# Kernel tuning notes

Hardware: AMD Instinct MI355X
Metric: run time of the kernel (lower is better)

Reference implementation:

```python
import jax, jax.numpy as jnp
import numpy as np

B, S, D = 4, 2048, 512
H, DK, DV = 8, 64, 64


def setup_inputs() -> dict:
    key = jax.random.key(0)
    ks = jax.random.split(key, 12)
    inv = 1.0 / np.sqrt(D)
    return {
        "query": jax.random.normal(ks[0], (B, S, D), dtype=jnp.float32),
        "value": jax.random.normal(ks[1], (B, S, D), dtype=jnp.float32),
        "attention_mask": jax.random.randint(ks[2], (B, S), 0, 2, dtype=jnp.int32),
        "Wq": jax.random.normal(ks[3], (D, H * DK), dtype=jnp.float32) * inv,
        "bq": jnp.zeros((H * DK,), dtype=jnp.float32),
        "Wk": jax.random.normal(ks[4], (D, H * DK), dtype=jnp.float32) * inv,
        "bk": jnp.zeros((H * DK,), dtype=jnp.float32),
        "Wv": jax.random.normal(ks[5], (D, H * DV), dtype=jnp.float32) * inv,
        "bv": jnp.zeros((H * DV,), dtype=jnp.float32),
        "Wo": jax.random.normal(ks[6], (H * DV, D), dtype=jnp.float32) * inv,
        "bo": jnp.zeros((D,), dtype=jnp.float32),
    }


def _split_heads(x, h):
    b, s, _ = x.shape
    return x.reshape(b, s, h, -1).transpose(0, 2, 1, 3)  # (B,H,S,dh)


def reference(query, value, attention_mask, Wq, bq, Wk, bk, Wv, bv, Wo, bo):
    # QKV projections (activation=None -> identity); key defaults to value
    q = _split_heads(query @ Wq + bq, H)   # (B,H,S,DK)
    k = _split_heads(value @ Wk + bk, H)   # (B,H,S,DK)
    v = _split_heads(value @ Wv + bv, H)   # (B,H,S,DV)

    scores = jnp.einsum("bhqd,bhkd->bhqk", q, k) / jnp.sqrt(jnp.float32(DK))
    # additive mask: m = 1e9*(mask-1), applied on both key and query axes
    m = 1e9 * (attention_mask.astype(jnp.float32) - 1.0)  # (B,S)
    scores = scores + m[:, None, None, :] + m[:, None, :, None]

    weights = jax.nn.softmax(scores, axis=-1)
    ctx = jnp.einsum("bhqk,bhkd->bhqd", weights, v)        # (B,H,S,DV)
    ctx = ctx.transpose(0, 2, 1, 3).reshape(ctx.shape[0], ctx.shape[2], H * DV)
    return ctx @ Wo + bo  # (B,S,D)
```

## Files before the change

### kernel.cpp

```cpp
#include <hip/hip_runtime.h>

#define B_ 4
#define S_ 2048
#define D_ 512
#define H_ 8

typedef __attribute__((ext_vector_type(8))) __bf16 bf16x8;
typedef __attribute__((ext_vector_type(4))) float f32x4;

#define NEGBIG  -1.442695040e9f
#define QSCALE  0.18033688011112042f

__device__ __forceinline__ unsigned pack_rn(float a, float b) {
    union { float f; unsigned u; } ua, ub; ua.f = a; ub.f = b;
    return __builtin_amdgcn_perm(ub.u + 0x8000u, ua.u + 0x8000u, 0x07060302u);
}

__device__ __forceinline__ void gl16(const void* g, void* l) {
    __builtin_amdgcn_global_load_lds(
        (const __attribute__((address_space(1))) unsigned int*)g,
        (__attribute__((address_space(3))) unsigned int*)l, 16, 0, 0);
}

__global__ __launch_bounds__(256) void pre_all(
    const float* __restrict__ q, const float* __restrict__ v,
    const int* __restrict__ am,
    const float* __restrict__ Wq, const float* __restrict__ Wk,
    const float* __restrict__ Wv, const float* __restrict__ Wo,
    unsigned short* __restrict__ xq, unsigned short* __restrict__ xv,
    unsigned short* __restrict__ Tq, unsigned short* __restrict__ Tk,
    unsigned short* __restrict__ Tv, unsigned short* __restrict__ To,
    int* __restrict__ idxc, int* __restrict__ nvout,
    float* __restrict__ Mf, float* __restrict__ Mc)
{
    const int bid = blockIdx.x;
    const int tid = threadIdx.x;

    if (bid < 4096) {
        const int z = bid >> 11, xb = bid & 2047;
        const float* src = z ? v : q;
        unsigned short* dst = z ? xv : xq;
        int i = (xb * 256 + tid) * 8;
        float4 f0 = *(const float4*)&src[i];
        float4 f1 = *(const float4*)&src[i + 4];
        uint4 o;
        o.x = pack_rn(f0.x, f0.y); o.y = pack_rn(f0.z, f0.w);
        o.z = pack_rn(f1.x, f1.y); o.w = pack_rn(f1.z, f1.w);
        *(uint4*)&dst[i] = o;
    } else if (bid < 4352) {
        int r = bid - 4096;
        int z = r >> 6, rem = r & 63;
        const float* W = (z == 0) ? Wq : (z == 1) ? Wk : (z == 2) ? Wv : Wo;
        unsigned short* T = (z == 0) ? Tq : (z == 1) ? Tk : (z == 2) ? Tv : To;
        int n0 = (rem & 7) * 64, k0 = (rem >> 3) * 64;

        __shared__ float Ts[64][69];
        #pragma unroll
        for (int it = 0; it < 4; it++) {
            int lin = tid + it * 256;
            int kr = lin >> 4, c4 = (lin & 15) * 4;
            float4 vv = *(const float4*)&W[(k0 + kr) * 512 + n0 + c4];
            Ts[kr][c4 + 0] = vv.x; Ts[kr][c4 + 1] = vv.y;
            Ts[kr][c4 + 2] = vv.z; Ts[kr][c4 + 3] = vv.w;
        }
        __syncthreads();
        int n = tid >> 2, kc = tid & 3;
        unsigned p[8];
        #pragma unroll
        for (int j = 0; j < 8; j++)
            p[j] = pack_rn(Ts[kc * 16 + 2 * j][n], Ts[kc * 16 + 2 * j + 1][n]);
        unsigned short* dst = &T[(n0 + n) * 512 + k0 + kc * 16];
        *(uint4*)dst       = *(uint4*)&p[0];
        *(uint4*)(dst + 8) = *(uint4*)&p[4];
    } else {
        const int w = tid >> 6, lane = tid & 63;
        const int* amb = am + w * 2048;
        int m[32];
        #pragma unroll
        for (int s = 0; s < 32; s++) m[s] = amb[s * 64 + lane];

        int* ib = idxc + w * 2048;
        const unsigned long long lt = (1ULL << lane) - 1ULL;
        int base = 0;
        #pragma unroll
        for (int s = 0; s < 32; s++) {
            unsigned long long bal = __ballot(m[s] != 0);
            if (m[s]) ib[base + __popcll(bal & lt)] = s * 64 + lane;
            base += __popcll(bal);
        }
        const int nv = base;
        for (int i = nv + lane; i < 2048; i += 64) ib[i] = 0;
        float* mfb = Mf + w * 2048;
        float* mcb = Mc + w * 2048;
        #pragma unroll
        for (int s = 0; s < 32; s++) {
            int i = s * 64 + lane;
            mfb[i] = m[s] ? 0.f : NEGBIG;
            mcb[i] = (i < nv) ? 0.f : NEGBIG;
        }
        if (lane == 0) nvout[w] = nv;
    }
}

__global__ __launch_bounds__(256) void proj_qkv_mfma(
    const unsigned short* __restrict__ Xq, const unsigned short* __restrict__ Xv,
    const unsigned short* __restrict__ Wtq, const unsigned short* __restrict__ Wtk,
    const unsigned short* __restrict__ Wtv,
    const float* __restrict__ bq, const float* __restrict__ bk,
    const float* __restrict__ bv,
    const int* __restrict__ idxc, const int* __restrict__ nv1,
    unsigned short* __restrict__ Qb, unsigned short* __restrict__ Kb,
    unsigned short* __restrict__ VtG)
{
    const int z = blockIdx.z;
    const unsigned short* A  = (z == 0) ? Wtq : (z == 1) ? Wtk : Xv;
    const unsigned short* Bm = (z == 0) ? Xq  : (z == 1) ? Xv  : Wtv;
    const float* bias        = (z == 0) ? bq  : (z == 1) ? bk  : bv;
    const int lin0 = blockIdx.y * 128 + blockIdx.x;
    const int m0 = (z < 2) ? blockIdx.y * 128 : (lin0 >> 3) * 128;
    const int n0 = (z < 2) ? blockIdx.x * 64  : (lin0 & 7) * 64;

    if (z == 1) {
        int bb = n0 >> 11, cap = (nv1[bb] + 63) & ~63;
        if (cap < 64) cap = 64;
        if ((n0 & 2047) >= cap) return;
    }
    if (z == 2) {
        int bb = m0 >> 11, cap = (nv1[bb] + 63) & ~63;
        if (cap < 64) cap = 64;
        if ((m0 & 2047) >= cap) return;
    }

    const int tid = threadIdx.x;
    const int w = tid >> 6, lane = tid & 63;
    const int l15 = lane & 15, quad = lane >> 4;
    const int wm = (w >> 1) * 64, wn = (w & 1) * 32;

    __shared__ unsigned short As[2][128 * 64];
    __shared__ unsigned short Bs[2][64 * 64];

    const int srw  = tid >> 3;
    const int csrc = (tid & 7) ^ (srw & 7);
    const unsigned short* aS[4];
    const unsigned short* bS[2];
    #pragma unroll
    for (int is = 0; is < 4; is++) {
        int ra = m0 + is * 32 + srw;
        long sa = ra;
        if (z == 2) { int bb = ra >> 11; sa = (long)bb * 2048 + idxc[bb * 2048 + (ra & 2047)]; }
        aS[is] = A + sa * 512 + csrc * 8;
    }
    #pragma unroll
    for (int is = 0; is < 2; is++) {
        int rb = n0 + is * 32 + srw;
        long sb = rb;
        if (z == 1) { int bb = rb >> 11; sb = (long)bb * 2048 + idxc[bb * 2048 + (rb & 2047)]; }
        bS[is] = Bm + sb * 512 + csrc * 8;
    }

    const int koff0 = ((quad    ) ^ (l15 & 7)) * 8;
    const int koff1 = ((quad + 4) ^ (l15 & 7)) * 8;

    f32x4 acc[4][2];
    #pragma unroll
    for (int i = 0; i < 4; i++)
        #pragma unroll
        for (int j = 0; j < 2; j++) acc[i][j] = (f32x4){0.f, 0.f, 0.f, 0.f};

    #define STAGE_Q(buf, k0)                                        \
        do {                                                        \
            _Pragma("unroll")                                       \
            for (int is = 0; is < 4; is++)                          \
                gl16(aS[is] + (k0), &As[buf][is * 2048 + w * 512]); \
            _Pragma("unroll")                                       \
            for (int is = 0; is < 2; is++)                          \
                gl16(bS[is] + (k0), &Bs[buf][is * 2048 + w * 512]); \
        } while (0)

    STAGE_Q(0, 0);
    for (int k = 0; k < 8; k++) {
        const int cur = k & 1;
        if (k < 7) {
            STAGE_Q(cur ^ 1, (k + 1) * 64);
            asm volatile("s_waitcnt vmcnt(6)" ::: "memory");
        } else {
            asm volatile("s_waitcnt vmcnt(0)" ::: "memory");
        }
        asm volatile("s_barrier" ::: "memory");
        #pragma unroll
        for (int kc = 0; kc < 2; kc++) {
            const int ko = kc ? koff1 : koff0;
            bf16x8 a[4], bb[2];
            #pragma unroll
            for (int i = 0; i < 4; i++)
                a[i] = *(const bf16x8*)&As[cur][(wm + 16 * i + l15) * 64 + ko];
            #pragma unroll
            for (int j = 0; j < 2; j++)
                bb[j] = *(const bf16x8*)&Bs[cur][(wn + 16 * j + l15) * 64 + ko];
            #pragma unroll
            for (int i = 0; i < 4; i++)
                #pragma unroll
                for (int j = 0; j < 2; j++)
                    acc[i][j] = __builtin_amdgcn_mfma_f32_16x16x32_bf16(a[i], bb[j], acc[i][j], 0, 0, 0);
        }
        asm volatile("s_barrier" ::: "memory");
    }
    #undef STAGE_Q

    if (z == 2) {
        #pragma unroll
        for (int j = 0; j < 2; j++) {
            int N = n0 + wn + 16 * j + l15;
            float bv_ = bias[N];
            int h = N >> 6, d = N & 63;
            #pragma unroll
            for (int i = 0; i < 4; i++) {
                int Mb = m0 + wm + 16 * i + quad * 4;
                int b = Mb >> 11, s = Mb & 2047;
                uint2 o;
                o.x = pack_rn(acc[i][j][0] + bv_, acc[i][j][1] + bv_);
                o.y = pack_rn(acc[i][j][2] + bv_, acc[i][j][3] + bv_);
                *(uint2*)&VtG[((b * H_ + h) * 64 + d) * 2048 + s] = o;
            }
        }
    } else {
        unsigned short* dst = (z == 0) ? Qb : Kb;
        const float scale = (z == 0) ? QSCALE : 1.0f;
        #pragma unroll
        for (int j = 0; j < 2; j++) {
            int sg = n0 + wn + 16 * j + l15;
            int b = sg >> 11, s = sg & 2047;
            #pragma unroll
            for (int i = 0; i < 4; i++) {
                int F = m0 + wm + 16 * i + quad * 4;
                int h = F >> 6, d = F & 63;
                float4 b4 = *(const float4*)&bias[F];
                uint2 o;
                o.x = pack_rn((acc[i][j][0] + b4.x) * scale, (acc[i][j][1] + b4.y) * scale);
                o.y = pack_rn((acc[i][j][2] + b4.z) * scale, (acc[i][j][3] + b4.w) * scale);
                *(uint2*)&dst[((b * H_ + h) * 2048 + s) * 64 + d] = o;
            }
        }
    }
}

__global__ __launch_bounds__(256, 2) void flash_mfma(
    const unsigned short* __restrict__ Qg, const unsigned short* __restrict__ Kg,
    const unsigned short* __restrict__ VtG, const float* __restrict__ Mf,
    const float* __restrict__ Mc, const int* __restrict__ nvalid,
    unsigned short* __restrict__ ctxB)
{
    const int bid = blockIdx.x;
    const int xcd = bid & 7, idx = bid >> 3;
    const int bh = xcd * 4 + (idx & 3);
    const int q0 = (idx >> 2) * 128;
    const int b = bh >> 3, h = bh & 7;

    const int tid = threadIdx.x;
    const int w = tid >> 6, lane = tid & 63;
    const int l15 = lane & 15, quad = lane >> 4;
    const int swz = l15 & 7;

    __shared__ unsigned short Ks[2][64 * 64];
    __shared__ unsigned short Ps[4][32 * 64];
    unsigned short* pw = &Ps[w][0];

    const int nv = nvalid[b];
    int ntiles = (nv + 63) >> 6;
    if (ntiles < 1) ntiles = 1;

    const float* mfb = Mf + b * 2048;
    const float* mcp = Mc + b * 2048 + quad * 4;

    bf16x8 qf[2][2];
    float mq[2];
    #pragma unroll
    for (int qb = 0; qb < 2; qb++) {
        int qrow = q0 + w * 32 + qb * 16 + l15;
        const unsigned short* p = &Qg[((long)bh * 2048 + qrow) * 64 + quad * 8];
        qf[qb][0] = *(const bf16x8*)p;
        qf[qb][1] = *(const bf16x8*)(p + 32);
        mq[qb] = mfb[qrow];
    }

    const unsigned short* vp[4];
    #pragma unroll
    for (int i = 0; i < 4; i++)
        vp[i] = VtG + ((long)bh * 64 + i * 16 + l15) * 2048 + quad * 8;

    const int srow = tid >> 2;
    const int sch  = (tid & 3) * 2;
    const unsigned short* kgb = Kg + (long)bh * 2048 * 64;
    const int sw0 = srow * 64 + ((sch    ) ^ (srow & 7)) * 8;
    const int sw1 = srow * 64 + ((sch + 1) ^ (srow & 7)) * 8;

    {
        uint4 a = *(const uint4*)&kgb[srow * 64 + sch * 8];
        uint4 c = *(const uint4*)&kgb[srow * 64 + sch * 8 + 8];
        *(uint4*)&Ks[0][sw0] = a;
        *(uint4*)&Ks[0][sw1] = c;
    }
    const int kt1 = (ntiles > 1) ? 64 : 0;
    uint4 kstA = *(const uint4*)&kgb[(kt1 + srow) * 64 + sch * 8];
    uint4 kstB = *(const uint4*)&kgb[(kt1 + srow) * 64 + sch * 8 + 8];

    const int koff0 = ((quad    ) ^ swz) * 8;
    const int koff1 = ((quad + 4) ^ swz) * 8;

    f32x4 accO[2][4];
    #pragma unroll
    for (int qb = 0; qb < 2; qb++)
        #pragma unroll
        for (int dt = 0; dt < 4; dt++) accO[qb][dt] = (f32x4){0.f, 0.f, 0.f, 0.f};
    float mi[2] = {-3.0e38f, -3.0e38f};
    float li[2] = {0.f, 0.f};

    __syncthreads();

    f32x4 scA[2][4], scB[2][4];
    {
        f32x4 kmf[4];
        #pragma unroll
        for (int nt = 0; nt < 4; nt++)
            kmf[nt] = *(const f32x4*)(mcp + nt * 16);
        bf16x8 kf[4][2];
        #pragma unroll
        for (int nt = 0; nt < 4; nt++) {
            kf[nt][0] = *(const bf16x8*)&Ks[0][(nt * 16 + l15) * 64 + koff0];
            kf[nt][1] = *(const bf16x8*)&Ks[0][(nt * 16 + l15) * 64 + koff1];
        }
        #pragma unroll
        for (int qb = 0; qb < 2; qb++)
            #pragma unroll
            for (int nt = 0; nt < 4; nt++) {
                f32x4 c = kmf[nt];
                c[0] += mq[qb]; c[1] += mq[qb]; c[2] += mq[qb]; c[3] += mq[qb];
                c = __builtin_amdgcn_mfma_f32_16x16x32_bf16(kf[nt][0], qf[qb][0], c, 0, 0, 0);
                c = __builtin_amdgcn_mfma_f32_16x16x32_bf16(kf[nt][1], qf[qb][1], c, 0, 0, 0);
                scA[qb][nt] = c;
            }
    }

    auto STEP = [&](f32x4 (&scCur)[2][4], f32x4 (&scNxt)[2][4], int t) {
        const int kt = t * 64;
        const int n = (t & 1) ^ 1;
        const bool hasNext = (t + 1 < ntiles);
        const int kt2 = (t + 2 < ntiles) ? (t + 2) * 64 : (ntiles - 1) * 64;

        bf16x8 vf[4][2];
        #pragma unroll
        for (int dt = 0; dt < 4; dt++) {
            vf[dt][0] = *(const bf16x8*)(vp[dt] + kt);
            vf[dt][1] = *(const bf16x8*)(vp[dt] + kt + 32);
        }
        uint4 k2A = *(const uint4*)&kgb[(kt2 + srow) * 64 + sch * 8];
        uint4 k2B = *(const uint4*)&kgb[(kt2 + srow) * 64 + sch * 8 + 8];
        f32x4 kmf[4];
        #pragma unroll
        for (int nt = 0; nt < 4; nt++)
            kmf[nt] = *(const f32x4*)(mcp + kt + 64 + nt * 16);

        *(uint4*)&Ks[n][sw0] = kstA;
        *(uint4*)&Ks[n][sw1] = kstB;
        __syncthreads();
        kstA = k2A; kstB = k2B;

        if (hasNext) {
            bf16x8 kf[4][2];
            #pragma unroll
            for (int nt = 0; nt < 4; nt++) {
                kf[nt][0] = *(const bf16x8*)&Ks[n][(nt * 16 + l15) * 64 + koff0];
                kf[nt][1] = *(const bf16x8*)&Ks[n][(nt * 16 + l15) * 64 + koff1];
            }
            #pragma unroll
            for (int qb = 0; qb < 2; qb++)
                #pragma unroll
                for (int nt = 0; nt < 4; nt++) {
                    f32x4 c = kmf[nt];
                    c[0] += mq[qb]; c[1] += mq[qb]; c[2] += mq[qb]; c[3] += mq[qb];
                    c = __builtin_amdgcn_mfma_f32_16x16x32_bf16(kf[nt][0], qf[qb][0], c, 0, 0, 0);
                    c = __builtin_amdgcn_mfma_f32_16x16x32_bf16(kf[nt][1], qf[qb][1], c, 0, 0, 0);
                    scNxt[qb][nt] = c;
                }
        }

        #pragma unroll
        for (int qb = 0; qb < 2; qb++) {
            float mloc = fmaxf(fmaxf(scCur[qb][0][0], scCur[qb][0][1]),
                               fmaxf(scCur[qb][0][2], scCur[qb][0][3]));
            #pragma unroll
            for (int nt = 1; nt < 4; nt++)
                mloc = fmaxf(mloc, fmaxf(fmaxf(scCur[qb][nt][0], scCur[qb][nt][1]),
                                         fmaxf(scCur[qb][nt][2], scCur[qb][nt][3])));
            mloc = fmaxf(mloc, __shfl_xor(mloc, 16));
            mloc = fmaxf(mloc, __shfl_xor(mloc, 32));

            float mn = mi[qb];
            if (!__all(mloc <= mn + 4.f)) {
                float mo = mn;
                mn = fmaxf(mo, mloc);
                float alpha = __builtin_amdgcn_exp2f(mo - mn);
                li[qb] *= alpha;
                #pragma unroll
                for (int dt = 0; dt < 4; dt++) {
                    accO[qb][dt][0] *= alpha; accO[qb][dt][1] *= alpha;
                    accO[qb][dt][2] *= alpha; accO[qb][dt][3] *= alpha;
                }
                mi[qb] = mn;
            }

            float ps = 0.f;
            const int prbase = (qb * 16 + l15) * 64;
            #pragma unroll
            for (int nt = 0; nt < 4; nt++) {
                float p0 = __builtin_amdgcn_exp2f(scCur[qb][nt][0] - mn);
                float p1 = __builtin_amdgcn_exp2f(scCur[qb][nt][1] - mn);
                float p2 = __builtin_amdgcn_exp2f(scCur[qb][nt][2] - mn);
                float p3 = __builtin_amdgcn_exp2f(scCur[qb][nt][3] - mn);
                ps += (p0 + p1) + (p2 + p3);
                uint2 pp;
                pp.x = pack_rn(p0, p1);
                pp.y = pack_rn(p2, p3);
                *(uint2*)&pw[prbase + ((2 * nt + (quad >> 1)) ^ swz) * 8 + (quad & 1) * 4] = pp;
            }
            ps += __shfl_xor(ps, 16);
            ps += __shfl_xor(ps, 32);
            li[qb] += ps;
        }

        #pragma unroll
        for (int qb = 0; qb < 2; qb++) {
            bf16x8 pf0 = *(const bf16x8*)&pw[(qb * 16 + l15) * 64 + koff0];
            bf16x8 pf1 = *(const bf16x8*)&pw[(qb * 16 + l15) * 64 + koff1];
            __builtin_amdgcn_s_setprio(1);
            #pragma unroll
            for (int dt = 0; dt < 4; dt++) {
                accO[qb][dt] = __builtin_amdgcn_mfma_f32_16x16x32_bf16(
                    vf[dt][0], pf0, accO[qb][dt], 0, 0, 0);
                accO[qb][dt] = __builtin_amdgcn_mfma_f32_16x16x32_bf16(
                    vf[dt][1], pf1, accO[qb][dt], 0, 0, 0);
            }
            __builtin_amdgcn_s_setprio(0);
        }
    };

    for (int t = 0; t < ntiles; t += 2) {
        STEP(scA, scB, t);
        if (t + 1 < ntiles) STEP(scB, scA, t + 1);
    }

    #pragma unroll
    for (int qb = 0; qb < 2; qb++) {
        float inv = 1.f / li[qb];
        int q = q0 + w * 32 + qb * 16 + l15;
        int obase = (b * 2048 + q) * 512 + h * 64 + quad * 4;
        #pragma unroll
        for (int dt = 0; dt < 4; dt++) {
            uint2 o;
            o.x = pack_rn(accO[qb][dt][0] * inv, accO[qb][dt][1] * inv);
            o.y = pack_rn(accO[qb][dt][2] * inv, accO[qb][dt][3] * inv);
            *(uint2*)&ctxB[obase + dt * 16] = o;
        }
    }
}

__global__ __launch_bounds__(256) void proj_out_mfma(
    const unsigned short* __restrict__ ctxB, const unsigned short* __restrict__ Wto,
    const float* __restrict__ bo, float* __restrict__ out)
{
    const int m0 = blockIdx.y * 128, n0 = blockIdx.x * 64;
    const int tid = threadIdx.x;
    const int w = tid >> 6, lane = tid & 63;
    const int l15 = lane & 15, quad = lane >> 4;
    const int wm = (w >> 1) * 64, wn = (w & 1) * 32;

    __shared__ unsigned short As[2][128 * 64];
    __shared__ unsigned short Bs[2][64 * 64];

    const int srw  = tid >> 3;
    const int csrc = (tid & 7) ^ (srw & 7);
    const unsigned short* aS[4];
    const unsigned short* bS[2];
    #pragma unroll
    for (int is = 0; is < 4; is++)
        aS[is] = Wto  + (long)(m0 + is * 32 + srw) * 512 + csrc * 8;
    #pragma unroll
    for (int is = 0; is < 2; is++)
        bS[is] = ctxB + (long)(n0 + is * 32 + srw) * 512 + csrc * 8;

    const int koff0 = ((quad    ) ^ (l15 & 7)) * 8;
    const int koff1 = ((quad + 4) ^ (l15 & 7)) * 8;

    f32x4 acc[4][2];
    #pragma unroll
    for (int i = 0; i < 4; i++)
        #pragma unroll
        for (int j = 0; j < 2; j++) acc[i][j] = (f32x4){0.f, 0.f, 0.f, 0.f};

    #define STAGE_O(buf, k0)                                        \
        do {                                                        \
            _Pragma("unroll")                                       \
            for (int is = 0; is < 4; is++)                          \
                gl16(aS[is] + (k0), &As[buf][is * 2048 + w * 512]); \
            _Pragma("unroll")                                       \
            for (int is = 0; is < 2; is++)                          \
                gl16(bS[is] + (k0), &Bs[buf][is * 2048 + w * 512]); \
        } while (0)

    STAGE_O(0, 0);
    for (int k = 0; k < 8; k++) {
        const int cur = k & 1;
        if (k < 7) {
            STAGE_O(cur ^ 1, (k + 1) * 64);
            asm volatile("s_waitcnt vmcnt(6)" ::: "memory");
        } else {
            asm volatile("s_waitcnt vmcnt(0)" ::: "memory");
        }
        asm volatile("s_barrier" ::: "memory");
        #pragma unroll
        for (int kc = 0; kc < 2; kc++) {
            const int ko = kc ? koff1 : koff0;
            bf16x8 a[4], bb[2];
            #pragma unroll
            for (int i = 0; i < 4; i++)
                a[i] = *(const bf16x8*)&As[cur][(wm + 16 * i + l15) * 64 + ko];
            #pragma unroll
            for (int j = 0; j < 2; j++)
                bb[j] = *(const bf16x8*)&Bs[cur][(wn + 16 * j + l15) * 64 + ko];
            #pragma unroll
            for (int i = 0; i < 4; i++)
                #pragma unroll
                for (int j = 0; j < 2; j++)
                    acc[i][j] = __builtin_amdgcn_mfma_f32_16x16x32_bf16(a[i], bb[j], acc[i][j], 0, 0, 0);
        }
        asm volatile("s_barrier" ::: "memory");
    }
    #undef STAGE_O

    #pragma unroll
    for (int j = 0; j < 2; j++) {
        int sg = n0 + wn + 16 * j + l15;
        #pragma unroll
        for (int i = 0; i < 4; i++) {
            int F = m0 + wm + 16 * i + quad * 4;
            float4 b4 = *(const float4*)&bo[F];
            float4 vv;
            vv.x = acc[i][j][0] + b4.x;
            vv.y = acc[i][j][1] + b4.y;
            vv.z = acc[i][j][2] + b4.z;
            vv.w = acc[i][j][3] + b4.w;
            *(float4*)&out[sg * 512 + F] = vv;
        }
    }
}

extern "C" void kernel_launch(void* const* d_in, const int* in_sizes, int n_in,
                              void* d_out, int out_size, void* d_ws, size_t ws_size,
                              hipStream_t stream)
{
    const float* query = (const float*)d_in[0];
    const float* value = (const float*)d_in[1];
    const int*   amask = (const int*)d_in[2];
    const float* Wq = (const float*)d_in[3];
    const float* bq = (const float*)d_in[4];
    const float* Wk = (const float*)d_in[5];
    const float* bk = (const float*)d_in[6];
    const float* Wv = (const float*)d_in[7];
    const float* bv = (const float*)d_in[8];
    const float* Wo = (const float*)d_in[9];
    const float* bo = (const float*)d_in[10];
    float* out = (float*)d_out;

    char* ws = (char*)d_ws;
    const size_t MB = 1 << 20;
    const size_t KB = 1 << 10;
    unsigned short* Xbq = (unsigned short*)(ws);
    unsigned short* Xbv = (unsigned short*)(ws + 8 * MB);
    unsigned short* Wtq = (unsigned short*)(ws + 16 * MB);
    unsigned short* Wtk = (unsigned short*)(ws + 16 * MB + MB / 2);
    unsigned short* Wtv = (unsigned short*)(ws + 17 * MB);
    unsigned short* Wto = (unsigned short*)(ws + 17 * MB + MB / 2);
    unsigned short* Qb  = (unsigned short*)(ws + 18 * MB);
    unsigned short* Kb  = (unsigned short*)(ws + 26 * MB);
    unsigned short* VtG = (unsigned short*)(ws + 34 * MB);
    int*   idx1 = (int*)(ws + 42 * MB);
    float* Mf   = (float*)(ws + 42 * MB + 32 * KB);
    float* Mc   = (float*)(ws + 42 * MB + 64 * KB);
    int*   nv   = (int*)(ws + 42 * MB + 96 * KB);
    unsigned short* ctx = Xbq;

    pre_all<<<dim3(4353), 256, 0, stream>>>(query, value, amask,
                                            Wq, Wk, Wv, Wo,
                                            Xbq, Xbv, Wtq, Wtk, Wtv, Wto,
                                            idx1, nv, Mf, Mc);
    proj_qkv_mfma<<<dim3(128, 4, 3), 256, 0, stream>>>(Xbq, Xbv, Wtq, Wtk, Wtv,
                                                       bq, bk, bv, idx1, nv,
                                                       Qb, Kb, VtG);
    flash_mfma<<<dim3(512), 256, 0, stream>>>(Qb, Kb, VtG, Mf, Mc, nv, ctx);
    proj_out_mfma<<<dim3(128, 4), 256, 0, stream>>>(ctx, Wto, bo, out);
}
```

Before: 180.3 us.

## Fuse fp32-to-bf16 activation conversion into QKV projection GEMM staging

Drops the separate pass in the preprocessing kernel that converted query and value to bf16 in workspace. The QKV projection kernel now loads fp32 activations through registers, packs them to bf16 and writes them into swizzled LDS, while weight tiles keep using async global-to-LDS loads. This saves a full read/write round trip of the activations, but each GEMM block reads twice the bytes for activations and register-staged loads plus __syncthreads replace the async-copy waits.

```diff
diff --git a/kernel.cpp b/kernel.cpp
--- a/kernel.cpp
+++ b/kernel.cpp
@@ -22,12 +22,10 @@
         (__attribute__((address_space(3))) unsigned int*)l, 16, 0, 0);
 }
 
-__global__ __launch_bounds__(256) void pre_all(
-    const float* __restrict__ q, const float* __restrict__ v,
+__global__ __launch_bounds__(256) void pre_small(
     const int* __restrict__ am,
     const float* __restrict__ Wq, const float* __restrict__ Wk,
     const float* __restrict__ Wv, const float* __restrict__ Wo,
-    unsigned short* __restrict__ xq, unsigned short* __restrict__ xv,
     unsigned short* __restrict__ Tq, unsigned short* __restrict__ Tk,
     unsigned short* __restrict__ Tv, unsigned short* __restrict__ To,
     int* __restrict__ idxc, int* __restrict__ nvout,
@@ -36,20 +34,8 @@
     const int bid = blockIdx.x;
     const int tid = threadIdx.x;
 
-    if (bid < 4096) {
-        const int z = bid >> 11, xb = bid & 2047;
-        const float* src = z ? v : q;
-        unsigned short* dst = z ? xv : xq;
-        int i = (xb * 256 + tid) * 8;
-        float4 f0 = *(const float4*)&src[i];
-        float4 f1 = *(const float4*)&src[i + 4];
-        uint4 o;
-        o.x = pack_rn(f0.x, f0.y); o.y = pack_rn(f0.z, f0.w);
-        o.z = pack_rn(f1.x, f1.y); o.w = pack_rn(f1.z, f1.w);
-        *(uint4*)&dst[i] = o;
-    } else if (bid < 4352) {
-        int r = bid - 4096;
-        int z = r >> 6, rem = r & 63;
+    if (bid < 256) {
+        int z = bid >> 6, rem = bid & 63;
         const float* W = (z == 0) ? Wq : (z == 1) ? Wk : (z == 2) ? Wv : Wo;
         unsigned short* T = (z == 0) ? Tq : (z == 1) ? Tk : (z == 2) ? Tv : To;
         int n0 = (rem & 7) * 64, k0 = (rem >> 3) * 64;
@@ -103,7 +89,7 @@
 }
 
 __global__ __launch_bounds__(256) void proj_qkv_mfma(
-    const unsigned short* __restrict__ Xq, const unsigned short* __restrict__ Xv,
+    const float* __restrict__ Xqf, const float* __restrict__ Xvf,
     const unsigned short* __restrict__ Wtq, const unsigned short* __restrict__ Wtk,
     const unsigned short* __restrict__ Wtv,
     const float* __restrict__ bq, const float* __restrict__ bk,
@@ -113,9 +99,7 @@
     unsigned short* __restrict__ VtG)
 {
     const int z = blockIdx.z;
-    const unsigned short* A  = (z == 0) ? Wtq : (z == 1) ? Wtk : Xv;
-    const unsigned short* Bm = (z == 0) ? Xq  : (z == 1) ? Xv  : Wtv;
-    const float* bias        = (z == 0) ? bq  : (z == 1) ? bk  : bv;
+    const float* bias = (z == 0) ? bq : (z == 1) ? bk : bv;
     const int lin0 = blockIdx.y * 128 + blockIdx.x;
     const int m0 = (z < 2) ? blockIdx.y * 128 : (lin0 >> 3) * 128;
     const int n0 = (z < 2) ? blockIdx.x * 64  : (lin0 & 7) * 64;
@@ -141,22 +125,53 @@
 
     const int srw  = tid >> 3;
     const int csrc = (tid & 7) ^ (srw & 7);
-    const unsigned short* aS[4];
-    const unsigned short* bS[2];
-    #pragma unroll
-    for (int is = 0; is < 4; is++) {
-        int ra = m0 + is * 32 + srw;
-        long sa = ra;
-        if (z == 2) { int bb = ra >> 11; sa = (long)bb * 2048 + idxc[bb * 2048 + (ra & 2047)]; }
-        aS[is] = A + sa * 512 + csrc * 8;
-    }
-    #pragma unroll
-    for (int is = 0; is < 2; is++) {
-        int rb = n0 + is * 32 + srw;
-        long sb = rb;
-        if (z == 1) { int bb = rb >> 11; sb = (long)bb * 2048 + idxc[bb * 2048 + (rb & 2047)]; }
-        bS[is] = Bm + sb * 512 + csrc * 8;
-    }
+    const unsigned short* gS[4];
+    unsigned short* gD[2][4];
+    int ngl;
+    if (z < 2) {
+        const unsigned short* Wt = (z == 0) ? Wtq : Wtk;
+        #pragma unroll
+        for (int is = 0; is < 4; is++) {
+            gS[is] = Wt + (long)(m0 + is * 32 + srw) * 512 + csrc * 8;
+            gD[0][is] = &As[0][is * 2048 + w * 512];
+            gD[1][is] = &As[1][is * 2048 + w * 512];
+        }
+        ngl = 4;
+    } else {
+        #pragma unroll
+        for (int is = 0; is < 2; is++) {
+            gS[is] = Wtv + (long)(n0 + is * 32 + srw) * 512 + csrc * 8;
+            gD[0][is] = &Bs[0][is * 2048 + w * 512];
+            gD[1][is] = &Bs[1][is * 2048 + w * 512];
+        }
+        gS[2] = gS[0]; gS[3] = gS[0];
+        gD[0][2] = gD[0][0]; gD[0][3] = gD[0][0];
+        gD[1][2] = gD[1][0]; gD[1][3] = gD[1][0];
+        ngl = 2;
+    }
+
+    const float* xsrc;
+    int xrow, cbase, nch;
+    if (z < 2) {
+        int rx = n0 + (tid >> 2);
+        long s = rx;
+        if (z == 1) { int bb = rx >> 11; s = (long)bb * 2048 + idxc[bb * 2048 + (rx & 2047)]; }
+        xsrc = ((z == 0) ? Xqf : Xvf) + s * 512;
+        xrow = tid >> 2; cbase = (tid & 3) * 2; nch = 2;
+    } else {
+        int rx = m0 + (tid >> 1);
+        int bb = rx >> 11;
+        long s = (long)bb * 2048 + idxc[bb * 2048 + (rx & 2047)];
+        xsrc = Xvf + s * 512;
+        xrow = tid >> 1; cbase = (tid & 1) * 4; nch = 4;
+    }
+    int xw[4];
+    #pragma unroll
+    for (int j = 0; j < 4; j++)
+        xw[j] = xrow * 64 + (((cbase + j) & 7) ^ (xrow & 7)) * 8;
+    unsigned short* xD[2];
+    xD[0] = (z < 2) ? &Bs[0][0] : &As[0][0];
+    xD[1] = (z < 2) ? &Bs[1][0] : &As[1][0];
 
     const int koff0 = ((quad    ) ^ (l15 & 7)) * 8;
     const int koff1 = ((quad + 4) ^ (l15 & 7)) * 8;
@@ -167,26 +182,43 @@
         #pragma unroll
         for (int j = 0; j < 2; j++) acc[i][j] = (f32x4){0.f, 0.f, 0.f, 0.f};
 
-    #define STAGE_Q(buf, k0)                                        \
-        do {                                                        \
-            _Pragma("unroll")                                       \
-            for (int is = 0; is < 4; is++)                          \
-                gl16(aS[is] + (k0), &As[buf][is * 2048 + w * 512]); \
-            _Pragma("unroll")                                       \
-            for (int is = 0; is < 2; is++)                          \
-                gl16(bS[is] + (k0), &Bs[buf][is * 2048 + w * 512]); \
-        } while (0)
-
-    STAGE_Q(0, 0);
+    float4 xr[4][2];
+
+    #pragma unroll
+    for (int j = 0; j < 4; j++)
+        if (j < nch) {
+            xr[j][0] = *(const float4*)(xsrc + (cbase + j) * 8);
+            xr[j][1] = *(const float4*)(xsrc + (cbase + j) * 8 + 4);
+        }
+    #pragma unroll
+    for (int is = 0; is < 4; is++)
+        if (is < ngl) gl16(gS[is], gD[0][is]);
+    #pragma unroll
+    for (int j = 0; j < 4; j++)
+        if (j < nch) {
+            uint4 p;
+            p.x = pack_rn(xr[j][0].x, xr[j][0].y);
+            p.y = pack_rn(xr[j][0].z, xr[j][0].w);
+            p.z = pack_rn(xr[j][1].x, xr[j][1].y);
+            p.w = pack_rn(xr[j][1].z, xr[j][1].w);
+            *(uint4*)&xD[0][xw[j]] = p;
+        }
+    __syncthreads();
+
     for (int k = 0; k < 8; k++) {
-        const int cur = k & 1;
+        const int cur = k & 1, nxt = cur ^ 1;
         if (k < 7) {
-            STAGE_Q(cur ^ 1, (k + 1) * 64);
-            asm volatile("s_waitcnt vmcnt(6)" ::: "memory");
-        } else {
-            asm volatile("s_waitcnt vmcnt(0)" ::: "memory");
-        }
-        asm volatile("s_barrier" ::: "memory");
+            const int k1 = (k + 1) * 64;
+            #pragma unroll
+            for (int j = 0; j < 4; j++)
+                if (j < nch) {
+                    xr[j][0] = *(const float4*)(xsrc + k1 + (cbase + j) * 8);
+                    xr[j][1] = *(const float4*)(xsrc + k1 + (cbase + j) * 8 + 4);
+                }
+            #pragma unroll
+            for (int is = 0; is < 4; is++)
+                if (is < ngl) gl16(gS[is] + k1, gD[nxt][is]);
+        }
         #pragma unroll
         for (int kc = 0; kc < 2; kc++) {
             const int ko = kc ? koff1 : koff0;
@@ -203,9 +235,20 @@
                 for (int j = 0; j < 2; j++)
                     acc[i][j] = __builtin_amdgcn_mfma_f32_16x16x32_bf16(a[i], bb[j], acc[i][j], 0, 0, 0);
         }
-        asm volatile("s_barrier" ::: "memory");
-    }
-    #undef STAGE_Q
+        if (k < 7) {
+            #pragma unroll
+            for (int j = 0; j < 4; j++)
+                if (j < nch) {
+                    uint4 p;
+                    p.x = pack_rn(xr[j][0].x, xr[j][0].y);
+                    p.y = pack_rn(xr[j][0].z, xr[j][0].w);
+                    p.z = pack_rn(xr[j][1].x, xr[j][1].y);
+                    p.w = pack_rn(xr[j][1].z, xr[j][1].w);
+                    *(uint4*)&xD[nxt][xw[j]] = p;
+                }
+        }
+        __syncthreads();
+    }
 
     if (z == 2) {
         #pragma unroll
@@ -574,8 +617,7 @@
     char* ws = (char*)d_ws;
     const size_t MB = 1 << 20;
     const size_t KB = 1 << 10;
-    unsigned short* Xbq = (unsigned short*)(ws);
-    unsigned short* Xbv = (unsigned short*)(ws + 8 * MB);
+    unsigned short* ctx = (unsigned short*)(ws);
     unsigned short* Wtq = (unsigned short*)(ws + 16 * MB);
     unsigned short* Wtk = (unsigned short*)(ws + 16 * MB + MB / 2);
     unsigned short* Wtv = (unsigned short*)(ws + 17 * MB);
@@ -587,13 +629,12 @@
     float* Mf   = (float*)(ws + 42 * MB + 32 * KB);
     float* Mc   = (float*)(ws + 42 * MB + 64 * KB);
     int*   nv   = (int*)(ws + 42 * MB + 96 * KB);
-    unsigned short* ctx = Xbq;
-
-    pre_all<<<dim3(4353), 256, 0, stream>>>(query, value, amask,
-                                            Wq, Wk, Wv, Wo,
-                                            Xbq, Xbv, Wtq, Wtk, Wtv, Wto,
-                                            idx1, nv, Mf, Mc);
-    proj_qkv_mfma<<<dim3(128, 4, 3), 256, 0, stream>>>(Xbq, Xbv, Wtq, Wtk, Wtv,
+
+    pre_small<<<dim3(257), 256, 0, stream>>>(amask, Wq, Wk, Wv, Wo,
+                                             Wtq, Wtk, Wtv, Wto,
+                                             idx1, nv, Mf, Mc);
+    proj_qkv_mfma<<<dim3(128, 4, 3), 256, 0, stream>>>(query, value,
+                                                       Wtq, Wtk, Wtv,
                                                        bq, bk, bv, idx1, nv,
                                                        Qb, Kb, VtG);
     flash_mfma<<<dim3(512), 256, 0, stream>>>(Qb, Kb, VtG, Mf, Mc, nv, ctx);
```

Measured after the change: 190.2 us. +5.5%, slower.

## Fuse four attention kernels into one persistent kernel with grid barriers

Applied to the files above, without the earlier changes.

Merges the preprocessing, QKV projection, flash attention and output projection kernels into a single persistent kernel of 512 blocks. The phases are separated by software grid barriers built on atomic counters in workspace, which are zeroed with a memset before launch. The goal is to remove the per-launch overhead and tail gaps between the kernels. In exchange, all 512 blocks must be co-resident, since the spin barriers can deadlock if they are not. Shared memory is also unified into one 48 KB buffer, and the barriers add spin and fence costs.

```diff
diff --git a/kernel.cpp b/kernel.cpp
--- a/kernel.cpp
+++ b/kernel.cpp
@@ -22,22 +22,40 @@
         (__attribute__((address_space(3))) unsigned int*)l, 16, 0, 0);
 }
 
-__global__ __launch_bounds__(256) void pre_all(
-    const float* __restrict__ q, const float* __restrict__ v,
-    const int* __restrict__ am,
-    const float* __restrict__ Wq, const float* __restrict__ Wk,
-    const float* __restrict__ Wv, const float* __restrict__ Wo,
-    unsigned short* __restrict__ xq, unsigned short* __restrict__ xv,
-    unsigned short* __restrict__ Tq, unsigned short* __restrict__ Tk,
-    unsigned short* __restrict__ Tv, unsigned short* __restrict__ To,
-    int* __restrict__ idxc, int* __restrict__ nvout,
-    float* __restrict__ Mf, float* __restrict__ Mc)
+struct MegaArgs {
+    const float *q, *v; const int* am;
+    const float *Wq, *Wk, *Wv, *Wo, *bq, *bk, *bv, *bo;
+    unsigned short *Xbq, *Xbv, *Tq, *Tk, *Tv, *To;
+    unsigned short *Qb, *Kb, *VtG, *ctx;
+    int *idxc, *nv; float *Mf, *Mc; float* out;
+    unsigned* bars;
+};
+
+#define NBLK 512u
+
+__device__ __forceinline__ void grid_bar(unsigned* cnt) {
+    asm volatile("s_waitcnt vmcnt(0) lgkmcnt(0)" ::: "memory");
+    __syncthreads();
+    if (threadIdx.x == 0) {
+        __threadfence_system();
+        __hip_atomic_fetch_add(cnt, 1u, __ATOMIC_RELEASE, __HIP_MEMORY_SCOPE_AGENT);
+        while (__hip_atomic_load(cnt, __ATOMIC_ACQUIRE, __HIP_MEMORY_SCOPE_AGENT) < NBLK)
+            __builtin_amdgcn_s_sleep(2);
+        __threadfence_system();
+    }
+    __syncthreads();
+}
+
+__device__ void phase_pre(char* smem, int it,
+    const float* q, const float* v, const int* am,
+    const float* Wq, const float* Wk, const float* Wv, const float* Wo,
+    unsigned short* xq, unsigned short* xv,
+    unsigned short* Tq, unsigned short* Tk, unsigned short* Tv, unsigned short* To,
+    int* idxc, int* nvout, float* Mf, float* Mc)
 {
-    const int bid = blockIdx.x;
     const int tid = threadIdx.x;
-
-    if (bid < 4096) {
-        const int z = bid >> 11, xb = bid & 2047;
+    if (it < 4096) {
+        const int z = it >> 11, xb = it & 2047;
         const float* src = z ? v : q;
         unsigned short* dst = z ? xv : xq;
         int i = (xb * 256 + tid) * 8;
@@ -47,28 +65,27 @@
         o.x = pack_rn(f0.x, f0.y); o.y = pack_rn(f0.z, f0.w);
         o.z = pack_rn(f1.x, f1.y); o.w = pack_rn(f1.z, f1.w);
         *(uint4*)&dst[i] = o;
-    } else if (bid < 4352) {
-        int r = bid - 4096;
+    } else if (it < 4352) {
+        int r = it - 4096;
         int z = r >> 6, rem = r & 63;
         const float* W = (z == 0) ? Wq : (z == 1) ? Wk : (z == 2) ? Wv : Wo;
         unsigned short* T = (z == 0) ? Tq : (z == 1) ? Tk : (z == 2) ? Tv : To;
         int n0 = (rem & 7) * 64, k0 = (rem >> 3) * 64;
-
-        __shared__ float Ts[64][69];
-        #pragma unroll
-        for (int it = 0; it < 4; it++) {
-            int lin = tid + it * 256;
+        float* Ts = (float*)smem;
+        #pragma unroll
+        for (int itr = 0; itr < 4; itr++) {
+            int lin = tid + itr * 256;
             int kr = lin >> 4, c4 = (lin & 15) * 4;
             float4 vv = *(const float4*)&W[(k0 + kr) * 512 + n0 + c4];
-            Ts[kr][c4 + 0] = vv.x; Ts[kr][c4 + 1] = vv.y;
-            Ts[kr][c4 + 2] = vv.z; Ts[kr][c4 + 3] = vv.w;
+            Ts[kr * 69 + c4 + 0] = vv.x; Ts[kr * 69 + c4 + 1] = vv.y;
+            Ts[kr * 69 + c4 + 2] = vv.z; Ts[kr * 69 + c4 + 3] = vv.w;
         }
         __syncthreads();
         int n = tid >> 2, kc = tid & 3;
         unsigned p[8];
         #pragma unroll
         for (int j = 0; j < 8; j++)
-            p[j] = pack_rn(Ts[kc * 16 + 2 * j][n], Ts[kc * 16 + 2 * j + 1][n]);
+            p[j] = pack_rn(Ts[(kc * 16 + 2 * j) * 69 + n], Ts[(kc * 16 + 2 * j + 1) * 69 + n]);
         unsigned short* dst = &T[(n0 + n) * 512 + k0 + kc * 16];
         *(uint4*)dst       = *(uint4*)&p[0];
         *(uint4*)(dst + 8) = *(uint4*)&p[4];
@@ -78,7 +95,6 @@
         int m[32];
         #pragma unroll
         for (int s = 0; s < 32; s++) m[s] = amb[s * 64 + lane];
-
         int* ib = idxc + w * 2048;
         const unsigned long long lt = (1ULL << lane) - 1ULL;
         int base = 0;
@@ -102,23 +118,18 @@
     }
 }
 
-__global__ __launch_bounds__(256) void proj_qkv_mfma(
-    const unsigned short* __restrict__ Xq, const unsigned short* __restrict__ Xv,
-    const unsigned short* __restrict__ Wtq, const unsigned short* __restrict__ Wtk,
-    const unsigned short* __restrict__ Wtv,
-    const float* __restrict__ bq, const float* __restrict__ bk,
-    const float* __restrict__ bv,
-    const int* __restrict__ idxc, const int* __restrict__ nv1,
-    unsigned short* __restrict__ Qb, unsigned short* __restrict__ Kb,
-    unsigned short* __restrict__ VtG)
+__device__ void phase_proj(char* smem, int z, int r,
+    const unsigned short* Xq, const unsigned short* Xv,
+    const unsigned short* Wtq, const unsigned short* Wtk, const unsigned short* Wtv,
+    const float* bq, const float* bk, const float* bv,
+    const int* idxc, const int* nv1,
+    unsigned short* Qb, unsigned short* Kb, unsigned short* VtG)
 {
-    const int z = blockIdx.z;
     const unsigned short* A  = (z == 0) ? Wtq : (z == 1) ? Wtk : Xv;
     const unsigned short* Bm = (z == 0) ? Xq  : (z == 1) ? Xv  : Wtv;
     const float* bias        = (z == 0) ? bq  : (z == 1) ? bk  : bv;
-    const int lin0 = blockIdx.y * 128 + blockIdx.x;
-    const int m0 = (z < 2) ? blockIdx.y * 128 : (lin0 >> 3) * 128;
-    const int n0 = (z < 2) ? blockIdx.x * 64  : (lin0 & 7) * 64;
+    const int m0 = (z < 2) ? (r >> 7) * 128 : (r >> 3) * 128;
+    const int n0 = (z < 2) ? (r & 127) * 64 : (r & 7) * 64;
 
     if (z == 1) {
         int bb = n0 >> 11, cap = (nv1[bb] + 63) & ~63;
@@ -131,13 +142,13 @@
         if ((m0 & 2047) >= cap) return;
     }
 
+    unsigned short* AsP = (unsigned short*)smem;
+    unsigned short* BsP = (unsigned short*)(smem + 32768);
+
     const int tid = threadIdx.x;
     const int w = tid >> 6, lane = tid & 63;
     const int l15 = lane & 15, quad = lane >> 4;
     const int wm = (w >> 1) * 64, wn = (w & 1) * 32;
-
-    __shared__ unsigned short As[2][128 * 64];
-    __shared__ unsigned short Bs[2][64 * 64];
 
     const int srw  = tid >> 3;
     const int csrc = (tid & 7) ^ (srw & 7);
@@ -167,14 +178,14 @@
         #pragma unroll
         for (int j = 0; j < 2; j++) acc[i][j] = (f32x4){0.f, 0.f, 0.f, 0.f};
 
-    #define STAGE_Q(buf, k0)                                        \
-        do {                                                        \
-            _Pragma("unroll")                                       \
-            for (int is = 0; is < 4; is++)                          \
-                gl16(aS[is] + (k0), &As[buf][is * 2048 + w * 512]); \
-            _Pragma("unroll")                                       \
-            for (int is = 0; is < 2; is++)                          \
-                gl16(bS[is] + (k0), &Bs[buf][is * 2048 + w * 512]); \
+    #define STAGE_Q(buf, k0)                                                   \
+        do {                                                                   \
+            _Pragma("unroll")                                                  \
+            for (int is = 0; is < 4; is++)                                     \
+                gl16(aS[is] + (k0), AsP + (buf) * 8192 + is * 2048 + w * 512); \
+            _Pragma("unroll")                                                  \
+            for (int is = 0; is < 2; is++)                                     \
+                gl16(bS[is] + (k0), BsP + (buf) * 4096 + is * 2048 + w * 512); \
         } while (0)
 
     STAGE_Q(0, 0);
@@ -193,10 +204,10 @@
             bf16x8 a[4], bb[2];
             #pragma unroll
             for (int i = 0; i < 4; i++)
-                a[i] = *(const bf16x8*)&As[cur][(wm + 16 * i + l15) * 64 + ko];
+                a[i] = *(const bf16x8*)&AsP[cur * 8192 + (wm + 16 * i + l15) * 64 + ko];
             #pragma unroll
             for (int j = 0; j < 2; j++)
-                bb[j] = *(const bf16x8*)&Bs[cur][(wn + 16 * j + l15) * 64 + ko];
+                bb[j] = *(const bf16x8*)&BsP[cur * 4096 + (wn + 16 * j + l15) * 64 + ko];
             #pragma unroll
             for (int i = 0; i < 4; i++)
                 #pragma unroll
@@ -244,13 +255,12 @@
     }
 }
 
-__global__ __launch_bounds__(256, 2) void flash_mfma(
-    const unsigned short* __restrict__ Qg, const unsigned short* __restrict__ Kg,
-    const unsigned short* __restrict__ VtG, const float* __restrict__ Mf,
-    const float* __restrict__ Mc, const int* __restrict__ nvalid,
-    unsigned short* __restrict__ ctxB)
+__device__ void phase_flash(char* smem, int bid,
+    const unsigned short* Qg, const unsigned short* Kg,
+    const unsigned short* VtG, const float* Mf,
+    const float* Mc, const int* nvalid,
+    unsigned short* ctxB)
 {
-    const int bid = blockIdx.x;
     const int xcd = bid & 7, idx = bid >> 3;
     const int bh = xcd * 4 + (idx & 3);
     const int q0 = (idx >> 2) * 128;
@@ -261,9 +271,8 @@
     const int l15 = lane & 15, quad = lane >> 4;
     const int swz = l15 & 7;
 
-    __shared__ unsigned short Ks[2][64 * 64];
-    __shared__ unsigned short Ps[4][32 * 64];
-    unsigned short* pw = &Ps[w][0];
+    unsigned short* KsP = (unsigned short*)smem;
+    unsigned short* pw  = (unsigned short*)(smem + 16384) + w * 2048;
 
     const int nv = nvalid[b];
     int ntiles = (nv + 63) >> 6;
@@ -297,8 +306,8 @@
     {
         uint4 a = *(const uint4*)&kgb[srow * 64 + sch * 8];
         uint4 c = *(const uint4*)&kgb[srow * 64 + sch * 8 + 8];
-        *(uint4*)&Ks[0][sw0] = a;
-        *(uint4*)&Ks[0][sw1] = c;
+        *(uint4*)&KsP[sw0] = a;
+        *(uint4*)&KsP[sw1] = c;
     }
     const int kt1 = (ntiles > 1) ? 64 : 0;
     uint4 kstA = *(const uint4*)&kgb[(kt1 + srow) * 64 + sch * 8];
@@ -326,8 +335,8 @@
         bf16x8 kf[4][2];
         #pragma unroll
         for (int nt = 0; nt < 4; nt++) {
-            kf[nt][0] = *(const bf16x8*)&Ks[0][(nt * 16 + l15) * 64 + koff0];
-            kf[nt][1] = *(const bf16x8*)&Ks[0][(nt * 16 + l15) * 64 + koff1];
+            kf[nt][0] = *(const bf16x8*)&KsP[(nt * 16 + l15) * 64 + koff0];
+            kf[nt][1] = *(const bf16x8*)&KsP[(nt * 16 + l15) * 64 + koff1];
         }
         #pragma unroll
         for (int qb = 0; qb < 2; qb++)
@@ -360,8 +369,8 @@
         for (int nt = 0; nt < 4; nt++)
             kmf[nt] = *(const f32x4*)(mcp + kt + 64 + nt * 16);
 
-        *(uint4*)&Ks[n][sw0] = kstA;
-        *(uint4*)&Ks[n][sw1] = kstB;
+        *(uint4*)&KsP[n * 4096 + sw0] = kstA;
+        *(uint4*)&KsP[n * 4096 + sw1] = kstB;
         __syncthreads();
         kstA = k2A; kstB = k2B;
 
@@ -369,8 +378,8 @@
             bf16x8 kf[4][2];
             #pragma unroll
             for (int nt = 0; nt < 4; nt++) {
-                kf[nt][0] = *(const bf16x8*)&Ks[n][(nt * 16 + l15) * 64 + koff0];
-                kf[nt][1] = *(const bf16x8*)&Ks[n][(nt * 16 + l15) * 64 + koff1];
+                kf[nt][0] = *(const bf16x8*)&KsP[n * 4096 + (nt * 16 + l15) * 64 + koff0];
+                kf[nt][1] = *(const bf16x8*)&KsP[n * 4096 + (nt * 16 + l15) * 64 + koff1];
             }
             #pragma unroll
             for (int qb = 0; qb < 2; qb++)
@@ -452,8 +461,8 @@
     #pragma unroll
     for (int qb = 0; qb < 2; qb++) {
         float inv = 1.f / li[qb];
-        int q = q0 + w * 32 + qb * 16 + l15;
-        int obase = (b * 2048 + q) * 512 + h * 64 + quad * 4;
+        int qq = q0 + w * 32 + qb * 16 + l15;
+        int obase = (b * 2048 + qq) * 512 + h * 64 + quad * 4;
         #pragma unroll
         for (int dt = 0; dt < 4; dt++) {
             uint2 o;
@@ -464,19 +473,19 @@
     }
 }
 
-__global__ __launch_bounds__(256) void proj_out_mfma(
-    const unsigned short* __restrict__ ctxB, const unsigned short* __restrict__ Wto,
-    const float* __restrict__ bo, float* __restrict__ out)
+__device__ void phase_out(char* smem, int r,
+    const unsigned short* ctxB, const unsigned short* Wto,
+    const float* bo, float* out)
 {
-    const int m0 = blockIdx.y * 128, n0 = blockIdx.x * 64;
+    const int m0 = (r >> 7) * 128, n0 = (r & 127) * 64;
+    unsigned short* AsP = (unsigned short*)smem;
+    unsigned short* BsP = (unsigned short*)(smem + 32768);
+
     const int tid = threadIdx.x;
     const int w = tid >> 6, lane = tid & 63;
     const int l15 = lane & 15, quad = lane >> 4;
     const int wm = (w >> 1) * 64, wn = (w & 1) * 32;
 
-    __shared__ unsigned short As[2][128 * 64];
-    __shared__ unsigned short Bs[2][64 * 64];
-
     const int srw  = tid >> 3;
     const int csrc = (tid & 7) ^ (srw & 7);
     const unsigned short* aS[4];
@@ -497,14 +506,14 @@
         #pragma unroll
         for (int j = 0; j < 2; j++) acc[i][j] = (f32x4){0.f, 0.f, 0.f, 0.f};
 
-    #define STAGE_O(buf, k0)                                        \
-        do {                                                        \
-            _Pragma("unroll")                                       \
-            for (int is = 0; is < 4; is++)                          \
-                gl16(aS[is] + (k0), &As[buf][is * 2048 + w * 512]); \
-            _Pragma("unroll")                                       \
-            for (int is = 0; is < 2; is++)                          \
-                gl16(bS[is] + (k0), &Bs[buf][is * 2048 + w * 512]); \
+    #define STAGE_O(buf, k0)                                                   \
+        do {                                                                   \
+            _Pragma("unroll")                                                  \
+            for (int is = 0; is < 4; is++)                                     \
+                gl16(aS[is] + (k0), AsP + (buf) * 8192 + is * 2048 + w * 512); \
+            _Pragma("unroll")                                                  \
+            for (int is = 0; is < 2; is++)                                     \
+                gl16(bS[is] + (k0), BsP + (buf) * 4096 + is * 2048 + w * 512); \
         } while (0)
 
     STAGE_O(0, 0);
@@ -523,10 +532,10 @@
             bf16x8 a[4], bb[2];
             #pragma unroll
             for (int i = 0; i < 4; i++)
-                a[i] = *(const bf16x8*)&As[cur][(wm + 16 * i + l15) * 64 + ko];
+                a[i] = *(const bf16x8*)&AsP[cur * 8192 + (wm + 16 * i + l15) * 64 + ko];
             #pragma unroll
             for (int j = 0; j < 2; j++)
-                bb[j] = *(const bf16x8*)&Bs[cur][(wn + 16 * j + l15) * 64 + ko];
+                bb[j] = *(const bf16x8*)&BsP[cur * 4096 + (wn + 16 * j + l15) * 64 + ko];
             #pragma unroll
             for (int i = 0; i < 4; i++)
                 #pragma unroll
@@ -554,48 +563,65 @@
     }
 }
 
+__global__ void __launch_bounds__(256, 2) mha_mega(MegaArgs a)
+{
+    __shared__ __align__(16) char smem[49152];
+    const int bid = blockIdx.x;
+
+    for (int it = bid; it < 4353; it += 512) {
+        phase_pre(smem, it, a.q, a.v, a.am, a.Wq, a.Wk, a.Wv, a.Wo,
+                  a.Xbq, a.Xbv, a.Tq, a.Tk, a.Tv, a.To, a.idxc, a.nv, a.Mf, a.Mc);
+        __syncthreads();
+    }
+    grid_bar(a.bars + 0);
+
+    for (int z = 0; z < 3; ++z) {
+        phase_proj(smem, z, bid, a.Xbq, a.Xbv, a.Tq, a.Tk, a.Tv,
+                   a.bq, a.bk, a.bv, a.idxc, a.nv, a.Qb, a.Kb, a.VtG);
+        __syncthreads();
+    }
+    grid_bar(a.bars + 16);
+
+    phase_flash(smem, bid, a.Qb, a.Kb, a.VtG, a.Mf, a.Mc, a.nv, a.ctx);
+    grid_bar(a.bars + 32);
+
+    phase_out(smem, bid, a.ctx, a.To, a.bo, a.out);
+}
+
 extern "C" void kernel_launch(void* const* d_in, const int* in_sizes, int n_in,
                               void* d_out, int out_size, void* d_ws, size_t ws_size,
                               hipStream_t stream)
 {
-    const float* query = (const float*)d_in[0];
-    const float* value = (const float*)d_in[1];
-    const int*   amask = (const int*)d_in[2];
-    const float* Wq = (const float*)d_in[3];
-    const float* bq = (const float*)d_in[4];
-    const float* Wk = (const float*)d_in[5];
-    const float* bk = (const float*)d_in[6];
-    const float* Wv = (const float*)d_in[7];
-    const float* bv = (const float*)d_in[8];
-    const float* Wo = (const float*)d_in[9];
-    const float* bo = (const float*)d_in[10];
-    float* out = (float*)d_out;
-
     char* ws = (char*)d_ws;
     const size_t MB = 1 << 20;
     const size_t KB = 1 << 10;
-    unsigned short* Xbq = (unsigned short*)(ws);
-    unsigned short* Xbv = (unsigned short*)(ws + 8 * MB);
-    unsigned short* Wtq = (unsigned short*)(ws + 16 * MB);
-    unsigned short* Wtk = (unsigned short*)(ws + 16 * MB + MB / 2);
-    unsigned short* Wtv = (unsigned short*)(ws + 17 * MB);
-    unsigned short* Wto = (unsigned short*)(ws + 17 * MB + MB / 2);
-    unsigned short* Qb  = (unsigned short*)(ws + 18 * MB);
-    unsigned short* Kb  = (unsigned short*)(ws + 26 * MB);
-    unsigned short* VtG = (unsigned short*)(ws + 34 * MB);
-    int*   idx1 = (int*)(ws + 42 * MB);
-    float* Mf   = (float*)(ws + 42 * MB + 32 * KB);
-    float* Mc   = (float*)(ws + 42 * MB + 64 * KB);
-    int*   nv   = (int*)(ws + 42 * MB + 96 * KB);
-    unsigned short* ctx = Xbq;
-
-    pre_all<<<dim3(4353), 256, 0, stream>>>(query, value, amask,
-                                            Wq, Wk, Wv, Wo,
-                                            Xbq, Xbv, Wtq, Wtk, Wtv, Wto,
-                                            idx1, nv, Mf, Mc);
-    proj_qkv_mfma<<<dim3(128, 4, 3), 256, 0, stream>>>(Xbq, Xbv, Wtq, Wtk, Wtv,
-                                                       bq, bk, bv, idx1, nv,
-                                                       Qb, Kb, VtG);
-    flash_mfma<<<dim3(512), 256, 0, stream>>>(Qb, Kb, VtG, Mf, Mc, nv, ctx);
-    proj_out_mfma<<<dim3(128, 4), 256, 0, stream>>>(ctx, Wto, bo, out);
-}
+
+    MegaArgs a;
+    a.q  = (const float*)d_in[0];
+    a.v  = (const float*)d_in[1];
+    a.am = (const int*)d_in[2];
+    a.Wq = (const float*)d_in[3];  a.bq = (const float*)d_in[4];
+    a.Wk = (const float*)d_in[5];  a.bk = (const float*)d_in[6];
+    a.Wv = (const float*)d_in[7];  a.bv = (const float*)d_in[8];
+    a.Wo = (const float*)d_in[9];  a.bo = (const float*)d_in[10];
+    a.out = (float*)d_out;
+
+    a.Xbq = (unsigned short*)(ws);
+    a.Xbv = (unsigned short*)(ws + 8 * MB);
+    a.Tq  = (unsigned short*)(ws + 16 * MB);
+    a.Tk  = (unsigned short*)(ws + 16 * MB + MB / 2);
+    a.Tv  = (unsigned short*)(ws + 17 * MB);
+    a.To  = (unsigned short*)(ws + 17 * MB + MB / 2);
+    a.Qb  = (unsigned short*)(ws + 18 * MB);
+    a.Kb  = (unsigned short*)(ws + 26 * MB);
+    a.VtG = (unsigned short*)(ws + 34 * MB);
+    a.idxc = (int*)(ws + 42 * MB);
+    a.Mf   = (float*)(ws + 42 * MB + 32 * KB);
+    a.Mc   = (float*)(ws + 42 * MB + 64 * KB);
+    a.nv   = (int*)(ws + 42 * MB + 96 * KB);
+    a.bars = (unsigned*)(ws + 42 * MB + 100 * KB);
+    a.ctx  = a.Xbq;
+
+    hipMemsetAsync(a.bars, 0, 256, stream);
+    mha_mega<<<dim3(512), dim3(256), 0, stream>>>(a);
+}
```

New measurement: 596.9 us. 231% more time.
